# Kernel optimization log

Measured on AMD Instinct MI355X. Metric: run time of the kernel, lower is better.

## Reference

```python
import jax, jax.numpy as jnp
import numpy as np

D = 512  # c_size == q_size


def setup_inputs() -> dict:
    key = jax.random.key(0)
    ks = jax.random.split(key, 8)
    c = jax.random.normal(ks[0], (8, 2048, D), dtype=jnp.float32)
    q = jax.random.normal(ks[1], (8, 512, D), dtype=jnp.float32)
    sc = 1.0 / np.sqrt(D)
    w_c = jax.random.uniform(ks[2], (D,), jnp.float32, -sc, sc)
    b_c = jax.random.uniform(ks[3], (), jnp.float32, -sc, sc)
    w_q = jax.random.uniform(ks[4], (D,), jnp.float32, -sc, sc)
    b_q = jax.random.uniform(ks[5], (), jnp.float32, -sc, sc)
    w_cq = jax.random.uniform(ks[6], (D,), jnp.float32, -sc, sc)
    b_cq = jax.random.uniform(ks[7], (), jnp.float32, -sc, sc)
    return {"c": c, "q": q, "w_c": w_c, "b_c": b_c, "w_q": w_q, "b_q": b_q,
            "w_cq": w_cq, "b_cq": b_cq}


def reference(c, q, w_c, b_c, w_q, b_q, w_cq, b_cq):
    # s[b,t,i] = <c[b,t],w_c>+b_c + <q[b,i],w_q>+b_q + <c[b,t]*q[b,i], w_cq>+b_cq
    # The original per-query-token loop for att_weight_cq(c*qi) collapses to
    # a single batched contraction since the Linear is linear in c*qi.
    sc = jnp.einsum('btd,d->bt', c, w_c) + b_c          # (B, c_len)
    sq = jnp.einsum('bid,d->bi', q, w_q) + b_q          # (B, q_len)
    scq = jnp.einsum('btd,bid->bti', c * w_cq, q) + b_cq  # (B, c_len, q_len)
    s = sc[:, :, None] + sq[:, None, :] + scq

    a = jax.nn.softmax(s, axis=2)                       # attend over q
    c2q = jnp.einsum('bti,bid->btd', a, q)              # (B, c_len, D)

    b = jax.nn.softmax(jnp.max(s, axis=2), axis=1)      # (B, c_len)
    q2c = jnp.einsum('bt,btd->bd', b, c)                # (B, D)
    q2c = jnp.broadcast_to(q2c[:, None, :], c.shape)    # (B, c_len, D)

    x = jnp.concatenate([c, c2q, c * c2q, c * q2c], axis=-1)
    return x
```

## Files before the change

kernel.cpp:

```cpp
#include <hip/hip_runtime.h>
#include <cstdint>


constexpr int kB = 8;
constexpr int kT = 2048;
constexpr int kI = 512;
constexpr int kD = 512;
constexpr int kW = 4 * kD;
constexpr int kRows = 64;
constexpr int kTiles = kT / kRows;
constexpr int kChunk = kRows * 72;

using f32x4  = __attribute__((ext_vector_type(4))) float;
using bf16x4 = __attribute__((ext_vector_type(4))) __bf16;
using bf16x8 = __attribute__((ext_vector_type(8))) __bf16;

__device__ __forceinline__ float wave_sum(float v) {
#pragma unroll
  for (int off = 32; off > 0; off >>= 1) v += __shfl_xor(v, off, 64);
  return v;
}
__device__ __forceinline__ float dot8(const f32x4& a0, const f32x4& a1,
                                      const f32x4& b0, const f32x4& b1) {
  return a0.x * b0.x + a0.y * b0.y + a0.z * b0.z + a0.w * b0.w +
         a1.x * b1.x + a1.y * b1.y + a1.z * b1.z + a1.w * b1.w;
}

__global__ __launch_bounds__(256) void prep_qf_kernel(
    const float* __restrict__ q, const float* __restrict__ w_q,
    const float* __restrict__ b_q, float* __restrict__ sq,
    __bf16* __restrict__ qf) {
  __shared__ float sacc[16][17];
  const int b = blockIdx.y;
  const int g = blockIdx.x;
  const int tid = threadIdx.x;
  const int kk0 = tid >> 6;
  const int lane = tid & 63;
  const int lr = lane & 15, lg = lane >> 4;
  const float* row = q + ((size_t)(b * kI + g * 16 + lr)) * kD;
  float sp = 0.f;
#pragma unroll
  for (int kk = kk0; kk < 16; kk += 4) {
    const int ka = kk * 32 + lg * 8;
    f32x4 v0 = *(const f32x4*)(row + ka);
    f32x4 v1 = *(const f32x4*)(row + ka + 4);
    f32x4 u0 = *(const f32x4*)(w_q + ka);
    f32x4 u1 = *(const f32x4*)(w_q + ka + 4);
    sp += dot8(v0, v1, u0, u1);
    bf16x8 o = {(__bf16)v0.x, (__bf16)v0.y, (__bf16)v0.z, (__bf16)v0.w,
                (__bf16)v1.x, (__bf16)v1.y, (__bf16)v1.z, (__bf16)v1.w};
    *(bf16x8*)(qf + ((((size_t)(b * 32 + g)) * 16 + kk) << 9) + lane * 8) = o;
  }
  sacc[lr][kk0 * 4 + lg] = sp;
  __syncthreads();
  if (tid < 16) {
    float s = 0.f;
#pragma unroll
    for (int j = 0; j < 16; ++j) s += sacc[tid][j];
    sq[b * kI + g * 16 + tid] = s + b_q[0];
  }
}

__global__ __launch_bounds__(256) void prep_vf_kernel(
    const float* __restrict__ q, __bf16* __restrict__ vf) {
  __shared__ float ts[64][68];
  const int b = blockIdx.z;
  const int i0 = blockIdx.x * 64;
  const int d0 = blockIdx.y * 64;
  const int tid = threadIdx.x;
  const int r = tid >> 2;
  const int cg = (tid & 3) * 16;
#pragma unroll
  for (int j = 0; j < 4; ++j) {
    f32x4 v = *(const f32x4*)(q + ((size_t)(b * kI + i0 + r)) * kD + d0 + cg + 4 * j);
    ts[r][cg + 4 * j + 0] = v.x;
    ts[r][cg + 4 * j + 1] = v.y;
    ts[r][cg + 4 * j + 2] = v.z;
    ts[r][cg + 4 * j + 3] = v.w;
  }
  __syncthreads();
  const int dl = tid >> 2;
  const int ig = (tid & 3) * 16;
  bf16x8 o0, o1;
#pragma unroll
  for (int j = 0; j < 8; ++j) o0[j] = (__bf16)ts[ig + j][dl];
#pragma unroll
  for (int j = 0; j < 8; ++j) o1[j] = (__bf16)ts[ig + 8 + j][dl];
  const int gd = (d0 >> 4) + (dl >> 4);
  const int lr = dl & 15;
  const int kki0 = (i0 >> 5) + (ig >> 5);
  const int lg0 = (ig & 31) >> 3;
  const int i1 = ig + 8;
  const int kki1 = (i0 >> 5) + (i1 >> 5);
  const int lg1 = (i1 & 31) >> 3;
  *(bf16x8*)(vf + ((((size_t)(b * 32 + gd)) * 16 + kki0) << 9) +
             (lg0 * 16 + lr) * 8) = o0;
  *(bf16x8*)(vf + ((((size_t)(b * 32 + gd)) * 16 + kki1) << 9) +
             (lg1 * 16 + lr) * 8) = o1;
}

__global__ __launch_bounds__(512, 2) void fused_attn(
    const float* __restrict__ c, const __bf16* __restrict__ qf,
    const __bf16* __restrict__ vf, const float* __restrict__ w_cq,
    const float* __restrict__ w_c, const float* __restrict__ b_c,
    const float* __restrict__ b_cq, const float* __restrict__ sq,
    float* __restrict__ out, float* __restrict__ mz,
    float* __restrict__ u_tile) {
  __shared__ __align__(16) char lAP[16 * kChunk];
  __shared__ float scrow[kRows];
  __shared__ float redm[8 * kRows];
  __shared__ float reds[8 * kRows];

  const int b = blockIdx.y;
  const int tile = blockIdx.x;
  const int t0 = tile * kRows;
  const int tid = threadIdx.x;
  const int w = tid >> 6;
  const int lane = tid & 63;
  const int lr = lane & 15, lg = lane >> 4;

  {
    const int srow = tid >> 3;
    const int col4 = (tid & 7) * 4;
    const float* crow = c + ((size_t)(b * kT + t0 + srow)) * kD;
    float scp = 0.f;
#pragma unroll
    for (int j = 0; j < 16; ++j) {
      const int col = col4 + j * 32;
      f32x4 v = *(const f32x4*)(crow + col);
      const f32x4 wq = *(const f32x4*)(w_cq + col);
      const f32x4 wc = *(const f32x4*)(w_c + col);
      scp += v.x * wc.x + v.y * wc.y + v.z * wc.z + v.w * wc.w;
      v *= wq;
      bf16x4 bv = {(__bf16)v.x, (__bf16)v.y, (__bf16)v.z, (__bf16)v.w};
      *(bf16x4*)(lAP + j * kChunk + srow * 72 + col4 * 2) = bv;
    }
    scp += __shfl_xor(scp, 1, 64);
    scp += __shfl_xor(scp, 2, 64);
    scp += __shfl_xor(scp, 4, 64);
    if ((tid & 7) == 0) scrow[srow] = scp + b_c[0];
  }
  __syncthreads();

  const __bf16* qfb = qf + (((size_t)(b * 32 + w * 4)) * 16 << 9) + lane * 8;
  f32x4 acc[4][4] = {};
  bf16x8 b0[4], b1[4], b2[4];
#pragma unroll
  for (int n4 = 0; n4 < 4; ++n4)
    b0[n4] = *(const bf16x8*)(qfb + (((size_t)(n4 * 16 + 0)) << 9));
#pragma unroll
  for (int n4 = 0; n4 < 4; ++n4)
    b1[n4] = *(const bf16x8*)(qfb + (((size_t)(n4 * 16 + 1)) << 9));
#pragma unroll
  for (int kk = 0; kk < 16; ++kk) {
    if (kk < 14) {
#pragma unroll
      for (int n4 = 0; n4 < 4; ++n4)
        b2[n4] = *(const bf16x8*)(qfb + (((size_t)(n4 * 16 + kk + 2)) << 9));
    }
    bf16x8 af[4];
#pragma unroll
    for (int m = 0; m < 4; ++m)
      af[m] = *(const bf16x8*)(lAP + kk * kChunk + (m * 16 + lr) * 72 + lg * 16);
#pragma unroll
    for (int m = 0; m < 4; ++m)
#pragma unroll
      for (int n4 = 0; n4 < 4; ++n4)
        acc[m][n4] = __builtin_amdgcn_mfma_f32_16x16x32_bf16(af[m], b0[n4],
                                                             acc[m][n4], 0, 0, 0);
#pragma unroll
    for (int n4 = 0; n4 < 4; ++n4) {
      b0[n4] = b1[n4];
      b1[n4] = b2[n4];
    }
  }

  const float bq = b_cq[0];
  float sqv[4];
#pragma unroll
  for (int n4 = 0; n4 < 4; ++n4) sqv[n4] = sq[b * kI + w * 64 + n4 * 16 + lr];
  float scr[4][4];
#pragma unroll
  for (int m = 0; m < 4; ++m)
#pragma unroll
    for (int r = 0; r < 4; ++r) scr[m][r] = scrow[m * 16 + lg * 4 + r] + bq;
#pragma unroll
  for (int m = 0; m < 4; ++m)
#pragma unroll
    for (int n4 = 0; n4 < 4; ++n4)
#pragma unroll
      for (int r = 0; r < 4; ++r) acc[m][n4][r] += scr[m][r] + sqv[n4];

  float mx[4][4];
#pragma unroll
  for (int m = 0; m < 4; ++m)
#pragma unroll
    for (int r = 0; r < 4; ++r) {
      float v = acc[m][0][r];
#pragma unroll
      for (int n4 = 1; n4 < 4; ++n4) v = fmaxf(v, acc[m][n4][r]);
#pragma unroll
      for (int off = 1; off <= 8; off <<= 1) v = fmaxf(v, __shfl_xor(v, off, 64));
      mx[m][r] = v;
    }
  if (lr == 0) {
#pragma unroll
    for (int m = 0; m < 4; ++m)
#pragma unroll
      for (int r = 0; r < 4; ++r)
        redm[w * kRows + m * 16 + lg * 4 + r] = mx[m][r];
  }
  __syncthreads();
#pragma unroll
  for (int m = 0; m < 4; ++m)
#pragma unroll
    for (int r = 0; r < 4; ++r) {
      const int rw = m * 16 + lg * 4 + r;
      float v = redm[rw];
#pragma unroll
      for (int w2 = 1; w2 < 8; ++w2) v = fmaxf(v, redm[w2 * kRows + rw]);
      mx[m][r] = v;
    }

  float sm[4][4] = {};
#pragma unroll
  for (int m = 0; m < 4; ++m)
#pragma unroll
    for (int n4 = 0; n4 < 4; ++n4)
#pragma unroll
      for (int r = 0; r < 4; ++r) {
        const float p = __expf(acc[m][n4][r] - mx[m][r]);
        acc[m][n4][r] = p;
        sm[m][r] += p;
      }
#pragma unroll
  for (int m = 0; m < 4; ++m)
#pragma unroll
    for (int r = 0; r < 4; ++r)
#pragma unroll
      for (int off = 1; off <= 8; off <<= 1)
        sm[m][r] += __shfl_xor(sm[m][r], off, 64);
  if (lr == 0) {
#pragma unroll
    for (int m = 0; m < 4; ++m)
#pragma unroll
      for (int r = 0; r < 4; ++r)
        reds[w * kRows + m * 16 + lg * 4 + r] = sm[m][r];
  }
  __syncthreads();
  float inv[4][4];
#pragma unroll
  for (int m = 0; m < 4; ++m)
#pragma unroll
    for (int r = 0; r < 4; ++r) {
      const int rw = m * 16 + lg * 4 + r;
      float v = reds[rw];
#pragma unroll
      for (int w2 = 1; w2 < 8; ++w2) v += reds[w2 * kRows + rw];
      inv[m][r] = 1.f / v;
    }

  const __bf16* vfb = vf + (((size_t)(b * 32 + w * 4)) * 16 << 9) + lane * 8;
  bf16x8 v0_[4], v1_[4], v2_[4];
#pragma unroll
  for (int n4 = 0; n4 < 4; ++n4)
    v0_[n4] = *(const bf16x8*)(vfb + (((size_t)(n4 * 16 + 0)) << 9));
#pragma unroll
  for (int n4 = 0; n4 < 4; ++n4)
    v1_[n4] = *(const bf16x8*)(vfb + (((size_t)(n4 * 16 + 1)) << 9));

#pragma unroll
  for (int m = 0; m < 4; ++m)
#pragma unroll
    for (int r = 0; r < 4; ++r) {
      const int trow = m * 16 + lg * 4 + r;
#pragma unroll
      for (int n4 = 0; n4 < 4; ++n4) {
        const int icol = w * 64 + n4 * 16 + lr;
        const int kkc = icol >> 5, kc = icol & 31;
        *(__bf16*)(lAP + kkc * kChunk + trow * 72 + kc * 2) =
            (__bf16)(acc[m][n4][r] * inv[m][r]);
      }
    }
  __syncthreads();

  f32x4 o[4][4] = {};
#pragma unroll
  for (int kki = 0; kki < 16; ++kki) {
    if (kki < 14) {
#pragma unroll
      for (int n4 = 0; n4 < 4; ++n4)
        v2_[n4] = *(const bf16x8*)(vfb + (((size_t)(n4 * 16 + kki + 2)) << 9));
    }
    bf16x8 af[4];
#pragma unroll
    for (int m = 0; m < 4; ++m)
      af[m] = *(const bf16x8*)(lAP + kki * kChunk + (m * 16 + lr) * 72 + lg * 16);
#pragma unroll
    for (int m = 0; m < 4; ++m)
#pragma unroll
      for (int n4 = 0; n4 < 4; ++n4)
        o[m][n4] = __builtin_amdgcn_mfma_f32_16x16x32_bf16(af[m], v0_[n4],
                                                           o[m][n4], 0, 0, 0);
#pragma unroll
    for (int n4 = 0; n4 < 4; ++n4) {
      v0_[n4] = v1_[n4];
      v1_[n4] = v2_[n4];
    }
  }

  float m_tile;
  {
    float v = mx[0][0];
#pragma unroll
    for (int m = 0; m < 4; ++m)
#pragma unroll
      for (int r = 0; r < 4; ++r) v = fmaxf(v, mx[m][r]);
    v = fmaxf(v, __shfl_xor(v, 16, 64));
    v = fmaxf(v, __shfl_xor(v, 32, 64));
    m_tile = v;
  }
  float u[4] = {};
  float zz = 0.f;
#pragma unroll
  for (int m = 0; m < 4; ++m)
#pragma unroll
    for (int r = 0; r < 4; ++r) {
      const int t = t0 + m * 16 + lg * 4 + r;
      const size_t rb = (size_t)(b * kT + t);
      const float* crow = c + rb * kD;
      float* orow = out + rb * kW;
      const float ev = __expf(mx[m][r] - m_tile);
      zz += ev;
#pragma unroll
      for (int n4 = 0; n4 < 4; ++n4) {
        const int d = w * 64 + n4 * 16 + lr;
        const float cvv = crow[d];
        const float pv = o[m][n4][r];
        orow[d] = cvv;
        orow[kD + d] = pv;
        orow[2 * kD + d] = cvv * pv;
        u[n4] += ev * cvv;
      }
    }
#pragma unroll
  for (int n4 = 0; n4 < 4; ++n4) {
    u[n4] += __shfl_xor(u[n4], 16, 64);
    u[n4] += __shfl_xor(u[n4], 32, 64);
  }
  if (lg == 0) {
    float* ub = u_tile + ((size_t)(b * kTiles + tile)) * kD;
#pragma unroll
    for (int n4 = 0; n4 < 4; ++n4) ub[w * 64 + n4 * 16 + lr] = u[n4];
  }
  if (w == 0) {
    zz += __shfl_xor(zz, 16, 64);
    zz += __shfl_xor(zz, 32, 64);
    if (lane == 0) {
      mz[b * 64 + tile] = m_tile;
      mz[b * 64 + 32 + tile] = zz;
    }
  }
}

__global__ __launch_bounds__(512) void merge_q2c_kernel(
    const float* __restrict__ mz, const float* __restrict__ u_tile,
    float* __restrict__ q2c) {
  const int b = blockIdx.x;
  const int d = threadIdx.x;
  __shared__ float sM[32], sZ[32];
  if (d < 32) {
    sM[d] = mz[b * 64 + d];
    sZ[d] = mz[b * 64 + 32 + d];
  }
  __syncthreads();
  float M = sM[0];
#pragma unroll
  for (int k = 1; k < 32; ++k) M = fmaxf(M, sM[k]);
  float Z = 0.f;
  float s = 0.f;
#pragma unroll
  for (int k = 0; k < 32; ++k) {
    const float wk = __expf(sM[k] - M);
    Z += wk * sZ[k];
    s += wk * u_tile[((size_t)(b * kTiles + k)) * kD + d];
  }
  q2c[b * kD + d] = s / Z;
}

__global__ __launch_bounds__(128) void slot3_kernel(
    const float* __restrict__ c, const float* __restrict__ q2c,
    float* __restrict__ out) {
  const int row = blockIdx.x;
  const int b = row >> 11;
  const int x4 = threadIdx.x * 4;
  f32x4 cv = *(const f32x4*)(c + (size_t)row * kD + x4);
  f32x4 qc = *(const f32x4*)(q2c + b * kD + x4);
  *(f32x4*)(out + (size_t)row * kW + 3 * kD + x4) = cv * qc;
}

extern "C" void kernel_launch(void* const* d_in, const int* in_sizes, int n_in,
                              void* d_out, int out_size, void* d_ws, size_t ws_size,
                              hipStream_t stream) {
  const float* c    = (const float*)d_in[0];
  const float* q    = (const float*)d_in[1];
  const float* w_c  = (const float*)d_in[2];
  const float* b_c  = (const float*)d_in[3];
  const float* w_q  = (const float*)d_in[4];
  const float* b_q  = (const float*)d_in[5];
  const float* w_cq = (const float*)d_in[6];
  const float* b_cq = (const float*)d_in[7];
  float* out = (float*)d_out;
  float* ws = (float*)d_ws;

  float* sq     = ws;
  float* q2c    = sq + kB * kI;
  float* mz     = q2c + kB * kD;
  float* u_tile = mz + kB * 64;
  __bf16* qf = (__bf16*)(u_tile + (size_t)kB * kTiles * kD);
  __bf16* vf = qf + (size_t)kB * kI * kD;

  dim3 gpq(kI / 16, kB);
  prep_qf_kernel<<<gpq, 256, 0, stream>>>(q, w_q, b_q, sq, qf);
  dim3 gpv(kI / 64, kD / 64, kB);
  prep_vf_kernel<<<gpv, 256, 0, stream>>>(q, vf);

  dim3 gf(kTiles, kB);
  fused_attn<<<gf, 512, 0, stream>>>(c, qf, vf, w_cq, w_c, b_c, b_cq, sq, out,
                                     mz, u_tile);

  merge_q2c_kernel<<<kB, 512, 0, stream>>>(mz, u_tile, q2c);
  slot3_kernel<<<kB * kT, 128, 0, stream>>>(c, q2c, out);
}
```

Measured before the change: 73.79 us.

## Use 1024-thread blocks with 16 waves splitting query/feature columns in fused attention

Doubles the fused attention workgroup to 16 waves, each owning 32 columns instead of 64, which halves per-wave accumulator registers and is meant to raise occupancy and latency hiding. The copy of c into the first output slot moves into the initial c-load pass as vectorized stores, and the cross-wave max/sum reductions are rewritten as a two-stage reduction through shared memory with extra barriers. The grid is linearized with batch in the low bits so that concurrently running blocks spread across batches. The trade-offs are more barriers and more waves reading the same shared-memory A tiles.

```diff
diff --git a/kernel.cpp b/kernel.cpp
--- a/kernel.cpp
+++ b/kernel.cpp
@@ -15,11 +15,6 @@
 using bf16x4 = __attribute__((ext_vector_type(4))) __bf16;
 using bf16x8 = __attribute__((ext_vector_type(8))) __bf16;
 
-__device__ __forceinline__ float wave_sum(float v) {
-#pragma unroll
-  for (int off = 32; off > 0; off >>= 1) v += __shfl_xor(v, off, 64);
-  return v;
-}
 __device__ __forceinline__ float dot8(const f32x4& a0, const f32x4& a1,
                                       const f32x4& b0, const f32x4& b1) {
   return a0.x * b0.x + a0.y * b0.y + a0.z * b0.z + a0.w * b0.w +
@@ -99,7 +94,7 @@
              (lg1 * 16 + lr) * 8) = o1;
 }
 
-__global__ __launch_bounds__(512, 2) void fused_attn(
+__global__ __launch_bounds__(1024, 4) void fused_attn(
     const float* __restrict__ c, const __bf16* __restrict__ qf,
     const __bf16* __restrict__ vf, const float* __restrict__ w_cq,
     const float* __restrict__ w_c, const float* __restrict__ b_c,
@@ -108,55 +103,59 @@
     float* __restrict__ u_tile) {
   __shared__ __align__(16) char lAP[16 * kChunk];
   __shared__ float scrow[kRows];
-  __shared__ float redm[8 * kRows];
-  __shared__ float reds[8 * kRows];
-
-  const int b = blockIdx.y;
-  const int tile = blockIdx.x;
+  __shared__ float redm[16 * kRows];
+  __shared__ float rfin[kRows];
+  __shared__ float sfin[kRows];
+
+  const int bid = blockIdx.x;
+  const int b = bid & 7;
+  const int tile = bid >> 3;
   const int t0 = tile * kRows;
   const int tid = threadIdx.x;
   const int w = tid >> 6;
   const int lane = tid & 63;
   const int lr = lane & 15, lg = lane >> 4;
 
+  const __bf16* qg0 = qf + (((size_t)(b * 32 + 2 * w + 0)) * 16 << 9) + lane * 8;
+  const __bf16* qg1 = qf + (((size_t)(b * 32 + 2 * w + 1)) * 16 << 9) + lane * 8;
+  bf16x8 b0[2], b1[2], b2[2];
+  b0[0] = *(const bf16x8*)(qg0);
+  b0[1] = *(const bf16x8*)(qg1);
+  b1[0] = *(const bf16x8*)(qg0 + (1 << 9));
+  b1[1] = *(const bf16x8*)(qg1 + (1 << 9));
+
   {
-    const int srow = tid >> 3;
-    const int col4 = (tid & 7) * 4;
+    const int srow = tid >> 4;
+    const int col4 = (tid & 15) * 4;
     const float* crow = c + ((size_t)(b * kT + t0 + srow)) * kD;
+    float* orow0 = out + ((size_t)(b * kT + t0 + srow)) * kW;
     float scp = 0.f;
 #pragma unroll
-    for (int j = 0; j < 16; ++j) {
-      const int col = col4 + j * 32;
+    for (int j = 0; j < 8; ++j) {
+      const int col = col4 + j * 64;
       f32x4 v = *(const f32x4*)(crow + col);
+      *(f32x4*)(orow0 + col) = v;
       const f32x4 wq = *(const f32x4*)(w_cq + col);
       const f32x4 wc = *(const f32x4*)(w_c + col);
       scp += v.x * wc.x + v.y * wc.y + v.z * wc.z + v.w * wc.w;
       v *= wq;
       bf16x4 bv = {(__bf16)v.x, (__bf16)v.y, (__bf16)v.z, (__bf16)v.w};
-      *(bf16x4*)(lAP + j * kChunk + srow * 72 + col4 * 2) = bv;
+      *(bf16x4*)(lAP + (col >> 5) * kChunk + srow * 72 + (col & 31) * 2) = bv;
     }
     scp += __shfl_xor(scp, 1, 64);
     scp += __shfl_xor(scp, 2, 64);
     scp += __shfl_xor(scp, 4, 64);
-    if ((tid & 7) == 0) scrow[srow] = scp + b_c[0];
-  }
-  __syncthreads();
-
-  const __bf16* qfb = qf + (((size_t)(b * 32 + w * 4)) * 16 << 9) + lane * 8;
-  f32x4 acc[4][4] = {};
-  bf16x8 b0[4], b1[4], b2[4];
-#pragma unroll
-  for (int n4 = 0; n4 < 4; ++n4)
-    b0[n4] = *(const bf16x8*)(qfb + (((size_t)(n4 * 16 + 0)) << 9));
-#pragma unroll
-  for (int n4 = 0; n4 < 4; ++n4)
-    b1[n4] = *(const bf16x8*)(qfb + (((size_t)(n4 * 16 + 1)) << 9));
+    scp += __shfl_xor(scp, 8, 64);
+    if ((tid & 15) == 0) scrow[srow] = scp + b_c[0];
+  }
+  __syncthreads();
+
+  f32x4 acc[4][2] = {};
 #pragma unroll
   for (int kk = 0; kk < 16; ++kk) {
     if (kk < 14) {
-#pragma unroll
-      for (int n4 = 0; n4 < 4; ++n4)
-        b2[n4] = *(const bf16x8*)(qfb + (((size_t)(n4 * 16 + kk + 2)) << 9));
+      b2[0] = *(const bf16x8*)(qg0 + ((size_t)(kk + 2) << 9));
+      b2[1] = *(const bf16x8*)(qg1 + ((size_t)(kk + 2) << 9));
     }
     bf16x8 af[4];
 #pragma unroll
@@ -165,20 +164,20 @@
 #pragma unroll
     for (int m = 0; m < 4; ++m)
 #pragma unroll
-      for (int n4 = 0; n4 < 4; ++n4)
-        acc[m][n4] = __builtin_amdgcn_mfma_f32_16x16x32_bf16(af[m], b0[n4],
-                                                             acc[m][n4], 0, 0, 0);
-#pragma unroll
-    for (int n4 = 0; n4 < 4; ++n4) {
-      b0[n4] = b1[n4];
-      b1[n4] = b2[n4];
+      for (int n = 0; n < 2; ++n)
+        acc[m][n] = __builtin_amdgcn_mfma_f32_16x16x32_bf16(af[m], b0[n],
+                                                            acc[m][n], 0, 0, 0);
+#pragma unroll
+    for (int n = 0; n < 2; ++n) {
+      b0[n] = b1[n];
+      b1[n] = b2[n];
     }
   }
 
   const float bq = b_cq[0];
-  float sqv[4];
-#pragma unroll
-  for (int n4 = 0; n4 < 4; ++n4) sqv[n4] = sq[b * kI + w * 64 + n4 * 16 + lr];
+  float sqv[2];
+#pragma unroll
+  for (int n = 0; n < 2; ++n) sqv[n] = sq[b * kI + w * 32 + n * 16 + lr];
   float scr[4][4];
 #pragma unroll
   for (int m = 0; m < 4; ++m)
@@ -187,18 +186,16 @@
 #pragma unroll
   for (int m = 0; m < 4; ++m)
 #pragma unroll
-    for (int n4 = 0; n4 < 4; ++n4)
-#pragma unroll
-      for (int r = 0; r < 4; ++r) acc[m][n4][r] += scr[m][r] + sqv[n4];
+    for (int n = 0; n < 2; ++n)
+#pragma unroll
+      for (int r = 0; r < 4; ++r) acc[m][n][r] += scr[m][r] + sqv[n];
 
   float mx[4][4];
 #pragma unroll
   for (int m = 0; m < 4; ++m)
 #pragma unroll
     for (int r = 0; r < 4; ++r) {
-      float v = acc[m][0][r];
-#pragma unroll
-      for (int n4 = 1; n4 < 4; ++n4) v = fmaxf(v, acc[m][n4][r]);
+      float v = fmaxf(acc[m][0][r], acc[m][1][r]);
 #pragma unroll
       for (int off = 1; off <= 8; off <<= 1) v = fmaxf(v, __shfl_xor(v, off, 64));
       mx[m][r] = v;
@@ -211,26 +208,27 @@
         redm[w * kRows + m * 16 + lg * 4 + r] = mx[m][r];
   }
   __syncthreads();
-#pragma unroll
-  for (int m = 0; m < 4; ++m)
-#pragma unroll
-    for (int r = 0; r < 4; ++r) {
-      const int rw = m * 16 + lg * 4 + r;
-      float v = redm[rw];
-#pragma unroll
-      for (int w2 = 1; w2 < 8; ++w2) v = fmaxf(v, redm[w2 * kRows + rw]);
-      mx[m][r] = v;
-    }
+  if (tid < kRows) {
+    float v = redm[tid];
+#pragma unroll
+    for (int w2 = 1; w2 < 16; ++w2) v = fmaxf(v, redm[w2 * kRows + tid]);
+    rfin[tid] = v;
+  }
+  __syncthreads();
+#pragma unroll
+  for (int m = 0; m < 4; ++m)
+#pragma unroll
+    for (int r = 0; r < 4; ++r) mx[m][r] = rfin[m * 16 + lg * 4 + r];
 
   float sm[4][4] = {};
 #pragma unroll
   for (int m = 0; m < 4; ++m)
 #pragma unroll
-    for (int n4 = 0; n4 < 4; ++n4)
+    for (int n = 0; n < 2; ++n)
 #pragma unroll
       for (int r = 0; r < 4; ++r) {
-        const float p = __expf(acc[m][n4][r] - mx[m][r]);
-        acc[m][n4][r] = p;
+        const float p = __expf(acc[m][n][r] - mx[m][r]);
+        acc[m][n][r] = p;
         sm[m][r] += p;
       }
 #pragma unroll
@@ -245,29 +243,29 @@
     for (int m = 0; m < 4; ++m)
 #pragma unroll
       for (int r = 0; r < 4; ++r)
-        reds[w * kRows + m * 16 + lg * 4 + r] = sm[m][r];
+        redm[w * kRows + m * 16 + lg * 4 + r] = sm[m][r];
+  }
+  __syncthreads();
+  if (tid < kRows) {
+    float v = redm[tid];
+#pragma unroll
+    for (int w2 = 1; w2 < 16; ++w2) v += redm[w2 * kRows + tid];
+    sfin[tid] = v;
   }
   __syncthreads();
   float inv[4][4];
 #pragma unroll
   for (int m = 0; m < 4; ++m)
 #pragma unroll
-    for (int r = 0; r < 4; ++r) {
-      const int rw = m * 16 + lg * 4 + r;
-      float v = reds[rw];
-#pragma unroll
-      for (int w2 = 1; w2 < 8; ++w2) v += reds[w2 * kRows + rw];
-      inv[m][r] = 1.f / v;
-    }
-
-  const __bf16* vfb = vf + (((size_t)(b * 32 + w * 4)) * 16 << 9) + lane * 8;
-  bf16x8 v0_[4], v1_[4], v2_[4];
-#pragma unroll
-  for (int n4 = 0; n4 < 4; ++n4)
-    v0_[n4] = *(const bf16x8*)(vfb + (((size_t)(n4 * 16 + 0)) << 9));
-#pragma unroll
-  for (int n4 = 0; n4 < 4; ++n4)
-    v1_[n4] = *(const bf16x8*)(vfb + (((size_t)(n4 * 16 + 1)) << 9));
+    for (int r = 0; r < 4; ++r) inv[m][r] = 1.f / sfin[m * 16 + lg * 4 + r];
+
+  const __bf16* vg0 = vf + (((size_t)(b * 32 + 2 * w + 0)) * 16 << 9) + lane * 8;
+  const __bf16* vg1 = vf + (((size_t)(b * 32 + 2 * w + 1)) * 16 << 9) + lane * 8;
+  bf16x8 v0_[2], v1_[2], v2_[2];
+  v0_[0] = *(const bf16x8*)(vg0);
+  v0_[1] = *(const bf16x8*)(vg1);
+  v1_[0] = *(const bf16x8*)(vg0 + (1 << 9));
+  v1_[1] = *(const bf16x8*)(vg1 + (1 << 9));
 
 #pragma unroll
   for (int m = 0; m < 4; ++m)
@@ -275,22 +273,19 @@
     for (int r = 0; r < 4; ++r) {
       const int trow = m * 16 + lg * 4 + r;
 #pragma unroll
-      for (int n4 = 0; n4 < 4; ++n4) {
-        const int icol = w * 64 + n4 * 16 + lr;
-        const int kkc = icol >> 5, kc = icol & 31;
-        *(__bf16*)(lAP + kkc * kChunk + trow * 72 + kc * 2) =
-            (__bf16)(acc[m][n4][r] * inv[m][r]);
+      for (int n = 0; n < 2; ++n) {
+        *(__bf16*)(lAP + w * kChunk + trow * 72 + (n * 16 + lr) * 2) =
+            (__bf16)(acc[m][n][r] * inv[m][r]);
       }
     }
   __syncthreads();
 
-  f32x4 o[4][4] = {};
+  f32x4 o[4][2] = {};
 #pragma unroll
   for (int kki = 0; kki < 16; ++kki) {
     if (kki < 14) {
-#pragma unroll
-      for (int n4 = 0; n4 < 4; ++n4)
-        v2_[n4] = *(const bf16x8*)(vfb + (((size_t)(n4 * 16 + kki + 2)) << 9));
+      v2_[0] = *(const bf16x8*)(vg0 + ((size_t)(kki + 2) << 9));
+      v2_[1] = *(const bf16x8*)(vg1 + ((size_t)(kki + 2) << 9));
     }
     bf16x8 af[4];
 #pragma unroll
@@ -299,13 +294,13 @@
 #pragma unroll
     for (int m = 0; m < 4; ++m)
 #pragma unroll
-      for (int n4 = 0; n4 < 4; ++n4)
-        o[m][n4] = __builtin_amdgcn_mfma_f32_16x16x32_bf16(af[m], v0_[n4],
-                                                           o[m][n4], 0, 0, 0);
-#pragma unroll
-    for (int n4 = 0; n4 < 4; ++n4) {
-      v0_[n4] = v1_[n4];
-      v1_[n4] = v2_[n4];
+      for (int n = 0; n < 2; ++n)
+        o[m][n] = __builtin_amdgcn_mfma_f32_16x16x32_bf16(af[m], v0_[n],
+                                                          o[m][n], 0, 0, 0);
+#pragma unroll
+    for (int n = 0; n < 2; ++n) {
+      v0_[n] = v1_[n];
+      v1_[n] = v2_[n];
     }
   }
 
@@ -320,7 +315,7 @@
     v = fmaxf(v, __shfl_xor(v, 32, 64));
     m_tile = v;
   }
-  float u[4] = {};
+  float u[2] = {};
   float zz = 0.f;
 #pragma unroll
   for (int m = 0; m < 4; ++m)
@@ -333,25 +328,24 @@
       const float ev = __expf(mx[m][r] - m_tile);
       zz += ev;
 #pragma unroll
-      for (int n4 = 0; n4 < 4; ++n4) {
-        const int d = w * 64 + n4 * 16 + lr;
+      for (int n = 0; n < 2; ++n) {
+        const int d = w * 32 + n * 16 + lr;
         const float cvv = crow[d];
-        const float pv = o[m][n4][r];
-        orow[d] = cvv;
+        const float pv = o[m][n][r];
         orow[kD + d] = pv;
         orow[2 * kD + d] = cvv * pv;
-        u[n4] += ev * cvv;
+        u[n] += ev * cvv;
       }
     }
 #pragma unroll
-  for (int n4 = 0; n4 < 4; ++n4) {
-    u[n4] += __shfl_xor(u[n4], 16, 64);
-    u[n4] += __shfl_xor(u[n4], 32, 64);
+  for (int n = 0; n < 2; ++n) {
+    u[n] += __shfl_xor(u[n], 16, 64);
+    u[n] += __shfl_xor(u[n], 32, 64);
   }
   if (lg == 0) {
     float* ub = u_tile + ((size_t)(b * kTiles + tile)) * kD;
 #pragma unroll
-    for (int n4 = 0; n4 < 4; ++n4) ub[w * 64 + n4 * 16 + lr] = u[n4];
+    for (int n = 0; n < 2; ++n) ub[w * 32 + n * 16 + lr] = u[n];
   }
   if (w == 0) {
     zz += __shfl_xor(zz, 16, 64);
@@ -425,9 +419,8 @@
   dim3 gpv(kI / 64, kD / 64, kB);
   prep_vf_kernel<<<gpv, 256, 0, stream>>>(q, vf);
 
-  dim3 gf(kTiles, kB);
-  fused_attn<<<gf, 512, 0, stream>>>(c, qf, vf, w_cq, w_c, b_c, b_cq, sq, out,
-                                     mz, u_tile);
+  fused_attn<<<kB * kTiles, 1024, 0, stream>>>(c, qf, vf, w_cq, w_c, b_c,
+                                               b_cq, sq, out, mz, u_tile);
 
   merge_q2c_kernel<<<kB, 512, 0, stream>>>(mz, u_tile, q2c);
   slot3_kernel<<<kB * kT, 128, 0, stream>>>(c, q2c, out);
```

New measurement: 74.67 us. No clear change (+1.2%).

## Fuse q2c merge and slot-3 write into attention kernel via cooperative grid sync

Applied to the files above, without the earlier changes.

Replaces the separate merge and slot-3 kernels with two grid-wide barriers inside a cooperatively launched attention kernel. Tile 0 of each batch merges the per-tile softmax statistics into q2c, then every block scales its own c rows, read back from slot 0 of the output, by q2c and writes slot 3. This is meant to save two launches and the extra full pass that re-read c for slot 3. The cost is two grid barriers, with most blocks idle while the merge runs, and the need for all 256 blocks to be co-resident.

```diff
diff --git a/kernel.cpp b/kernel.cpp
--- a/kernel.cpp
+++ b/kernel.cpp
@@ -1,6 +1,9 @@
 #include <hip/hip_runtime.h>
+#include <hip/hip_cooperative_groups.h>
 #include <cstdint>
 
+
+namespace cg = cooperative_groups;
 
 constexpr int kB = 8;
 constexpr int kT = 2048;
@@ -15,11 +18,6 @@
 using bf16x4 = __attribute__((ext_vector_type(4))) __bf16;
 using bf16x8 = __attribute__((ext_vector_type(8))) __bf16;
 
-__device__ __forceinline__ float wave_sum(float v) {
-#pragma unroll
-  for (int off = 32; off > 0; off >>= 1) v += __shfl_xor(v, off, 64);
-  return v;
-}
 __device__ __forceinline__ float dot8(const f32x4& a0, const f32x4& a1,
                                       const f32x4& b0, const f32x4& b1) {
   return a0.x * b0.x + a0.y * b0.y + a0.z * b0.z + a0.w * b0.w +
@@ -69,14 +67,14 @@
   const int d0 = blockIdx.y * 64;
   const int tid = threadIdx.x;
   const int r = tid >> 2;
-  const int cg = (tid & 3) * 16;
+  const int cg2 = (tid & 3) * 16;
 #pragma unroll
   for (int j = 0; j < 4; ++j) {
-    f32x4 v = *(const f32x4*)(q + ((size_t)(b * kI + i0 + r)) * kD + d0 + cg + 4 * j);
-    ts[r][cg + 4 * j + 0] = v.x;
-    ts[r][cg + 4 * j + 1] = v.y;
-    ts[r][cg + 4 * j + 2] = v.z;
-    ts[r][cg + 4 * j + 3] = v.w;
+    f32x4 v = *(const f32x4*)(q + ((size_t)(b * kI + i0 + r)) * kD + d0 + cg2 + 4 * j);
+    ts[r][cg2 + 4 * j + 0] = v.x;
+    ts[r][cg2 + 4 * j + 1] = v.y;
+    ts[r][cg2 + 4 * j + 2] = v.z;
+    ts[r][cg2 + 4 * j + 3] = v.w;
   }
   __syncthreads();
   const int dl = tid >> 2;
@@ -99,17 +97,18 @@
              (lg1 * 16 + lr) * 8) = o1;
 }
 
-__global__ __launch_bounds__(512, 2) void fused_attn(
+__global__ __launch_bounds__(512, 2) void fused_all(
     const float* __restrict__ c, const __bf16* __restrict__ qf,
     const __bf16* __restrict__ vf, const float* __restrict__ w_cq,
     const float* __restrict__ w_c, const float* __restrict__ b_c,
     const float* __restrict__ b_cq, const float* __restrict__ sq,
     float* __restrict__ out, float* __restrict__ mz,
-    float* __restrict__ u_tile) {
+    float* __restrict__ u_tile, float* __restrict__ q2c) {
   __shared__ __align__(16) char lAP[16 * kChunk];
   __shared__ float scrow[kRows];
   __shared__ float redm[8 * kRows];
   __shared__ float reds[8 * kRows];
+  __shared__ float sq2c[kD];
 
   const int b = blockIdx.y;
   const int tile = blockIdx.x;
@@ -361,42 +360,44 @@
       mz[b * 64 + 32 + tile] = zz;
     }
   }
-}
-
-__global__ __launch_bounds__(512) void merge_q2c_kernel(
-    const float* __restrict__ mz, const float* __restrict__ u_tile,
-    float* __restrict__ q2c) {
-  const int b = blockIdx.x;
-  const int d = threadIdx.x;
-  __shared__ float sM[32], sZ[32];
-  if (d < 32) {
-    sM[d] = mz[b * 64 + d];
-    sZ[d] = mz[b * 64 + 32 + d];
-  }
-  __syncthreads();
-  float M = sM[0];
-#pragma unroll
-  for (int k = 1; k < 32; ++k) M = fmaxf(M, sM[k]);
-  float Z = 0.f;
-  float s = 0.f;
-#pragma unroll
-  for (int k = 0; k < 32; ++k) {
-    const float wk = __expf(sM[k] - M);
-    Z += wk * sZ[k];
-    s += wk * u_tile[((size_t)(b * kTiles + k)) * kD + d];
-  }
-  q2c[b * kD + d] = s / Z;
-}
-
-__global__ __launch_bounds__(128) void slot3_kernel(
-    const float* __restrict__ c, const float* __restrict__ q2c,
-    float* __restrict__ out) {
-  const int row = blockIdx.x;
-  const int b = row >> 11;
-  const int x4 = threadIdx.x * 4;
-  f32x4 cv = *(const f32x4*)(c + (size_t)row * kD + x4);
-  f32x4 qc = *(const f32x4*)(q2c + b * kD + x4);
-  *(f32x4*)(out + (size_t)row * kW + 3 * kD + x4) = cv * qc;
+
+  cg::this_grid().sync();
+  if (tile == 0) {
+    if (tid < 32) {
+      redm[tid] = mz[b * 64 + tid];
+      redm[32 + tid] = mz[b * 64 + 32 + tid];
+    }
+    __syncthreads();
+    float M = redm[0];
+#pragma unroll
+    for (int k = 1; k < 32; ++k) M = fmaxf(M, redm[k]);
+    float Z = 0.f;
+    float s = 0.f;
+#pragma unroll
+    for (int k = 0; k < 32; ++k) {
+      const float wk = __expf(redm[k] - M);
+      Z += wk * redm[32 + k];
+      s += wk * u_tile[((size_t)(b * kTiles + k)) * kD + tid];
+    }
+    q2c[b * kD + tid] = s / Z;
+  }
+  cg::this_grid().sync();
+
+  sq2c[tid] = q2c[b * kD + tid];
+  __syncthreads();
+  {
+    const int srow = tid >> 3;
+    const int col4 = (tid & 7) * 4;
+    const size_t rb = (size_t)(b * kT + t0 + srow);
+    float* orow = out + rb * kW;
+#pragma unroll
+    for (int j = 0; j < 16; ++j) {
+      const int col = col4 + j * 32;
+      const f32x4 cv = *(const f32x4*)(orow + col);
+      const f32x4 qc = *(const f32x4*)(sq2c + col);
+      *(f32x4*)(orow + 3 * kD + col) = cv * qc;
+    }
+  }
 }
 
 extern "C" void kernel_launch(void* const* d_in, const int* in_sizes, int n_in,
@@ -425,10 +426,9 @@
   dim3 gpv(kI / 64, kD / 64, kB);
   prep_vf_kernel<<<gpv, 256, 0, stream>>>(q, vf);
 
-  dim3 gf(kTiles, kB);
-  fused_attn<<<gf, 512, 0, stream>>>(c, qf, vf, w_cq, w_c, b_c, b_cq, sq, out,
-                                     mz, u_tile);
-
-  merge_q2c_kernel<<<kB, 512, 0, stream>>>(mz, u_tile, q2c);
-  slot3_kernel<<<kB * kT, 128, 0, stream>>>(c, q2c, out);
+  void* args[] = {(void*)&c,    (void*)&qf,   (void*)&vf,  (void*)&w_cq,
+                  (void*)&w_c,  (void*)&b_c,  (void*)&b_cq, (void*)&sq,
+                  (void*)&out,  (void*)&mz,   (void*)&u_tile, (void*)&q2c};
+  hipLaunchCooperativeKernel((void*)fused_all, dim3(kTiles, kB), dim3(512),
+                             args, 0, stream);
 }
```

After: 148.6 us. 2.01x slower.

## Interleave c-tile staging with QK MFMA loop and fuse q2c merge into slot3

Applied to the files above, without the earlier changes.

The c rows are no longer staged into LDS in a prologue before the score GEMM. Each k-chunk is now loaded, scaled and written to LDS inside the MFMA loop, one chunk ahead, with a barrier per iteration. The slot-0 copy of c is written during that staging, and the epilogue re-reads c from the output buffer. The separate merge_q2c and slot3 kernels become one kernel per tile: each block recomputes q2c into shared memory and then writes slot 3. This removes one launch and hides the c load latency behind the MFMAs, at the cost of 16 barriers and redundant per-block merge work.

```diff
diff --git a/kernel.cpp b/kernel.cpp
--- a/kernel.cpp
+++ b/kernel.cpp
@@ -15,11 +15,6 @@
 using bf16x4 = __attribute__((ext_vector_type(4))) __bf16;
 using bf16x8 = __attribute__((ext_vector_type(8))) __bf16;
 
-__device__ __forceinline__ float wave_sum(float v) {
-#pragma unroll
-  for (int off = 32; off > 0; off >>= 1) v += __shfl_xor(v, off, 64);
-  return v;
-}
 __device__ __forceinline__ float dot8(const f32x4& a0, const f32x4& a1,
                                       const f32x4& b0, const f32x4& b1) {
   return a0.x * b0.x + a0.y * b0.y + a0.z * b0.z + a0.w * b0.w +
@@ -119,28 +114,24 @@
   const int lane = tid & 63;
   const int lr = lane & 15, lg = lane >> 4;
 
+  const int srow = tid >> 3;
+  const int col4 = (tid & 7) * 4;
+  const float* crow = c + ((size_t)(b * kT + t0 + srow)) * kD;
+  float* orow0 = out + ((size_t)(b * kT + t0 + srow)) * kW;
+  float scp = 0.f;
+
+  f32x4 c1, c2;
   {
-    const int srow = tid >> 3;
-    const int col4 = (tid & 7) * 4;
-    const float* crow = c + ((size_t)(b * kT + t0 + srow)) * kD;
-    float scp = 0.f;
-#pragma unroll
-    for (int j = 0; j < 16; ++j) {
-      const int col = col4 + j * 32;
-      f32x4 v = *(const f32x4*)(crow + col);
-      const f32x4 wq = *(const f32x4*)(w_cq + col);
-      const f32x4 wc = *(const f32x4*)(w_c + col);
-      scp += v.x * wc.x + v.y * wc.y + v.z * wc.z + v.w * wc.w;
-      v *= wq;
-      bf16x4 bv = {(__bf16)v.x, (__bf16)v.y, (__bf16)v.z, (__bf16)v.w};
-      *(bf16x4*)(lAP + j * kChunk + srow * 72 + col4 * 2) = bv;
-    }
-    scp += __shfl_xor(scp, 1, 64);
-    scp += __shfl_xor(scp, 2, 64);
-    scp += __shfl_xor(scp, 4, 64);
-    if ((tid & 7) == 0) scrow[srow] = scp + b_c[0];
-  }
-  __syncthreads();
+    f32x4 c0 = *(const f32x4*)(crow + col4);
+    c1 = *(const f32x4*)(crow + 32 + col4);
+    const f32x4 wq = *(const f32x4*)(w_cq + col4);
+    const f32x4 wc = *(const f32x4*)(w_c + col4);
+    *(f32x4*)(orow0 + col4) = c0;
+    scp += c0.x * wc.x + c0.y * wc.y + c0.z * wc.z + c0.w * wc.w;
+    c0 *= wq;
+    bf16x4 bv = {(__bf16)c0.x, (__bf16)c0.y, (__bf16)c0.z, (__bf16)c0.w};
+    *(bf16x4*)(lAP + 0 * kChunk + srow * 72 + col4 * 2) = bv;
+  }
 
   const __bf16* qfb = qf + (((size_t)(b * 32 + w * 4)) * 16 << 9) + lane * 8;
   f32x4 acc[4][4] = {};
@@ -151,8 +142,11 @@
 #pragma unroll
   for (int n4 = 0; n4 < 4; ++n4)
     b1[n4] = *(const bf16x8*)(qfb + (((size_t)(n4 * 16 + 1)) << 9));
+  __syncthreads();
+
 #pragma unroll
   for (int kk = 0; kk < 16; ++kk) {
+    if (kk < 14) c2 = *(const f32x4*)(crow + (kk + 2) * 32 + col4);
     if (kk < 14) {
 #pragma unroll
       for (int n4 = 0; n4 < 4; ++n4)
@@ -168,12 +162,30 @@
       for (int n4 = 0; n4 < 4; ++n4)
         acc[m][n4] = __builtin_amdgcn_mfma_f32_16x16x32_bf16(af[m], b0[n4],
                                                              acc[m][n4], 0, 0, 0);
+    if (kk < 15) {
+      const int col = (kk + 1) * 32 + col4;
+      const f32x4 wq = *(const f32x4*)(w_cq + col);
+      const f32x4 wc = *(const f32x4*)(w_c + col);
+      *(f32x4*)(orow0 + col) = c1;
+      scp += c1.x * wc.x + c1.y * wc.y + c1.z * wc.z + c1.w * wc.w;
+      f32x4 vv = c1 * wq;
+      bf16x4 bv = {(__bf16)vv.x, (__bf16)vv.y, (__bf16)vv.z, (__bf16)vv.w};
+      *(bf16x4*)(lAP + (kk + 1) * kChunk + srow * 72 + col4 * 2) = bv;
+      c1 = c2;
+    }
 #pragma unroll
     for (int n4 = 0; n4 < 4; ++n4) {
       b0[n4] = b1[n4];
       b1[n4] = b2[n4];
     }
-  }
+    __syncthreads();
+  }
+
+  scp += __shfl_xor(scp, 1, 64);
+  scp += __shfl_xor(scp, 2, 64);
+  scp += __shfl_xor(scp, 4, 64);
+  if ((tid & 7) == 0) scrow[srow] = scp + b_c[0];
+  __syncthreads();
 
   const float bq = b_cq[0];
   float sqv[4];
@@ -328,16 +340,14 @@
     for (int r = 0; r < 4; ++r) {
       const int t = t0 + m * 16 + lg * 4 + r;
       const size_t rb = (size_t)(b * kT + t);
-      const float* crow = c + rb * kD;
       float* orow = out + rb * kW;
       const float ev = __expf(mx[m][r] - m_tile);
       zz += ev;
 #pragma unroll
       for (int n4 = 0; n4 < 4; ++n4) {
         const int d = w * 64 + n4 * 16 + lr;
-        const float cvv = crow[d];
+        const float cvv = orow[d];
         const float pv = o[m][n4][r];
-        orow[d] = cvv;
         orow[kD + d] = pv;
         orow[2 * kD + d] = cvv * pv;
         u[n4] += ev * cvv;
@@ -363,40 +373,47 @@
   }
 }
 
-__global__ __launch_bounds__(512) void merge_q2c_kernel(
-    const float* __restrict__ mz, const float* __restrict__ u_tile,
-    float* __restrict__ q2c) {
-  const int b = blockIdx.x;
-  const int d = threadIdx.x;
+__global__ __launch_bounds__(512) void slot3_merge_kernel(
+    const float* __restrict__ c, const float* __restrict__ mz,
+    const float* __restrict__ u_tile, float* __restrict__ out) {
+  const int b = blockIdx.y;
+  const int tile = blockIdx.x;
+  const int t0 = tile * kRows;
+  const int tid = threadIdx.x;
   __shared__ float sM[32], sZ[32];
-  if (d < 32) {
-    sM[d] = mz[b * 64 + d];
-    sZ[d] = mz[b * 64 + 32 + d];
-  }
-  __syncthreads();
-  float M = sM[0];
-#pragma unroll
-  for (int k = 1; k < 32; ++k) M = fmaxf(M, sM[k]);
-  float Z = 0.f;
-  float s = 0.f;
-#pragma unroll
-  for (int k = 0; k < 32; ++k) {
-    const float wk = __expf(sM[k] - M);
-    Z += wk * sZ[k];
-    s += wk * u_tile[((size_t)(b * kTiles + k)) * kD + d];
-  }
-  q2c[b * kD + d] = s / Z;
-}
-
-__global__ __launch_bounds__(128) void slot3_kernel(
-    const float* __restrict__ c, const float* __restrict__ q2c,
-    float* __restrict__ out) {
-  const int row = blockIdx.x;
-  const int b = row >> 11;
-  const int x4 = threadIdx.x * 4;
-  f32x4 cv = *(const f32x4*)(c + (size_t)row * kD + x4);
-  f32x4 qc = *(const f32x4*)(q2c + b * kD + x4);
-  *(f32x4*)(out + (size_t)row * kW + 3 * kD + x4) = cv * qc;
+  __shared__ float sq2c[kD];
+  if (tid < 32) {
+    sM[tid] = mz[b * 64 + tid];
+    sZ[tid] = mz[b * 64 + 32 + tid];
+  }
+  __syncthreads();
+  {
+    float M = sM[0];
+#pragma unroll
+    for (int k = 1; k < 32; ++k) M = fmaxf(M, sM[k]);
+    float Z = 0.f;
+    float s = 0.f;
+#pragma unroll
+    for (int k = 0; k < 32; ++k) {
+      const float wk = __expf(sM[k] - M);
+      Z += wk * sZ[k];
+      s += wk * u_tile[((size_t)(b * kTiles + k)) * kD + tid];
+    }
+    sq2c[tid] = s / Z;
+  }
+  __syncthreads();
+  const int srow = tid >> 3;
+  const int col4 = (tid & 7) * 4;
+  const size_t rb = (size_t)(b * kT + t0 + srow);
+  const float* crow = c + rb * kD;
+  float* orow3 = out + rb * kW + 3 * kD;
+#pragma unroll
+  for (int j = 0; j < 16; ++j) {
+    const int col = col4 + j * 32;
+    const f32x4 cv = *(const f32x4*)(crow + col);
+    const f32x4 qc = *(const f32x4*)(sq2c + col);
+    *(f32x4*)(orow3 + col) = cv * qc;
+  }
 }
 
 extern "C" void kernel_launch(void* const* d_in, const int* in_sizes, int n_in,
@@ -414,8 +431,7 @@
   float* ws = (float*)d_ws;
 
   float* sq     = ws;
-  float* q2c    = sq + kB * kI;
-  float* mz     = q2c + kB * kD;
+  float* mz     = sq + kB * kI;
   float* u_tile = mz + kB * 64;
   __bf16* qf = (__bf16*)(u_tile + (size_t)kB * kTiles * kD);
   __bf16* vf = qf + (size_t)kB * kI * kD;
@@ -429,6 +445,5 @@
   fused_attn<<<gf, 512, 0, stream>>>(c, qf, vf, w_cq, w_c, b_c, b_cq, sq, out,
                                      mz, u_tile);
 
-  merge_q2c_kernel<<<kB, 512, 0, stream>>>(mz, u_tile, q2c);
-  slot3_kernel<<<kB * kT, 128, 0, stream>>>(c, q2c, out);
-}
+  slot3_merge_kernel<<<gf, 512, 0, stream>>>(c, mz, u_tile, out);
+}
```

Result: no change. 72.92 us (-1.2%).
